# Kernel optimization log

Hardware: AMD Instinct MI355X
Metric: run time of the kernel (lower is better)

Reference implementation:

```python
import jax, jax.numpy as jnp
import numpy as np

B, N1, N2, D, L, H = 2, 384, 384, 128, 3, 128
DM_MIN = 0.5


def _gat_layer(x, adj, W, Wb, A, gW, gb):
    # GAT_gate from jaechanglim/DTI_PDBbind: attention softmax over dim 1, gated residual
    h = x @ W + Wb                                   # [B,N,D]
    e = jnp.einsum('bjl,bkl->bjk', h @ A, h)
    e = e + jnp.swapaxes(e, 1, 2)
    att = jnp.where(adj > 0, e, -9e15)
    att = jax.nn.softmax(att, axis=1) * adj
    h_prime = jax.nn.relu(jnp.einsum('bij,bjk->bik', att, h))
    coeff = jax.nn.sigmoid(jnp.concatenate([x, h_prime], -1) @ gW + gb)  # [B,N,1]
    return coeff * x + (1.0 - coeff) * h_prime


def _pair_mlp(h1g, h2g, W1, b1, W2, b2):
    # MLP(concat(h1_i, h2_j)) without materializing the [B,N1,N2,2D] concat:
    # split W1 into ligand / protein halves and broadcast-add the projections.
    p1 = jnp.einsum('bnd,dk->bnk', h1g, W1[:D])      # [B,N1,H]
    p2 = jnp.einsum('bmd,dk->bmk', h2g, W1[D:])      # [B,N2,H]
    hid = jax.nn.relu(p1[:, :, None, :] + p2[:, None, :, :] + b1)  # [B,N1,N2,H]
    return (hid @ W2 + b2)[..., 0]                   # [B,N1,N2]


def reference(h1, adj1, h2, dmv, charge1, charge2, vdw_epsilon, vdw_sigma,
              delta_uff, valid1, valid2, no_metal1, no_metal2,
              node_W, gat_W, gat_Wb, gat_A, gat_gW, gat_gb,
              pair_W1, pair_b1, pair_W2, pair_b2,
              vdw_coeff, duff_coeff, int_W1, int_b1, int_W2, int_b2):
    h1g = h1 @ node_W
    h2g = h2 @ node_W
    for i in range(L):  # only ligand graph is convolved (as in the source)
        h1g = _gat_layer(h1g, adj1, gat_W[i], gat_Wb[i], gat_A[i], gat_gW[i], gat_gb[i])

    dm = jnp.sqrt(jnp.sum(dmv * dmv, -1) + 1e-10)    # [B,N1,N2]
    dm = jnp.where(dm < DM_MIN, 1e10, dm)

    # coulomb term (pair MLPs 0,1)
    cA = jax.nn.sigmoid(_pair_mlp(h1g, h2g, pair_W1[0], pair_b1[0], pair_W2[0], pair_b2[0]))
    cN = jax.nn.sigmoid(_pair_mlp(h1g, h2g, pair_W1[1], pair_b1[1], pair_W2[1], pair_b2[1])) * 2.0 + 1.0
    charge12 = charge1[:, :, None] * charge2[:, None, :]
    e_c = cA * charge12 * jnp.power(1.0 / dm, cN)
    e_c = e_c * valid1[:, :, None] * valid2[:, None, :]
    e_c = jnp.clip(e_c, -100.0, 100.0)
    e_c = jnp.sum(e_c, axis=(1, 2))[:, None]

    # vdw term (pair MLPs 2=A sigmoid, 3=B tanh, 4=N sigmoid)
    vA = (jax.nn.sigmoid(_pair_mlp(h1g, h2g, pair_W1[2], pair_b1[2], pair_W2[2], pair_b2[2])) * 0.6 + 0.7)
    vA = vA * (vdw_coeff[0] * vdw_coeff[0]) * vdw_epsilon
    vB = jnp.tanh(_pair_mlp(h1g, h2g, pair_W1[3], pair_b1[3], pair_W2[3], pair_b2[3])) * 0.6 + 0.7
    vN = jax.nn.sigmoid(_pair_mlp(h1g, h2g, pair_W1[4], pair_b1[4], pair_W2[4], pair_b2[4])) * 2.0 + 5.0
    dm0 = vdw_sigma * vB
    dm0 = jnp.where(dm0 < 1e-4, 1.0, dm0)
    r = jnp.power(dm0 / dm, vN)
    e_v = vA * (r * r - 2.0 * r)                     # (dm0/dm)^(2N) - 2(dm0/dm)^N
    e_v = e_v * no_metal1[:, :, None] * no_metal2[:, None, :]
    e_v = jnp.minimum(e_v, 100.0)
    e_v = jnp.sum(e_v, axis=(1, 2))[:, None]

    # conformational energy difference term
    e_u = (duff_coeff[0] * duff_coeff[0] * delta_uff)[:, None]

    # learned intercept from pooled ligand features
    hs = jnp.sum(h1g * valid1[..., None], axis=1)
    inter = jax.nn.relu(hs @ int_W1 + int_b1) @ int_W2 + int_b2

    return jnp.concatenate([e_c, e_v, e_u, inter], -1)  # [B,4]


def setup_inputs() -> dict:
    key = jax.random.key(0)
    ks = jax.random.split(key, 24)
    inp = {}
    inp['h1'] = jax.random.normal(ks[0], (B, N1, 54), jnp.float32)
    inp['h2'] = jax.random.normal(ks[1], (B, N2, 54), jnp.float32)
    a = jax.random.uniform(ks[2], (B, N1, N1))
    adj = (a > 0.9).astype(jnp.float32)
    adj = jnp.maximum(adj, jnp.swapaxes(adj, 1, 2))
    inp['adj1'] = jnp.maximum(adj, jnp.eye(N1, dtype=jnp.float32)[None])
    inp['dmv'] = jax.random.normal(ks[3], (B, N1, N2, 3), jnp.float32) * 3.0
    inp['charge1'] = jax.random.normal(ks[4], (B, N1), jnp.float32) * 0.3
    inp['charge2'] = jax.random.normal(ks[5], (B, N2), jnp.float32) * 0.3
    inp['vdw_epsilon'] = jax.random.uniform(ks[6], (B, N1, N2), jnp.float32) * 0.3
    inp['vdw_sigma'] = 3.0 + jax.random.uniform(ks[7], (B, N1, N2), jnp.float32)
    inp['delta_uff'] = jax.random.uniform(ks[8], (B,), jnp.float32) * 5.0
    inp['valid1'] = jnp.ones((B, N1), jnp.float32)
    inp['valid2'] = jnp.ones((B, N2), jnp.float32)
    inp['no_metal1'] = jnp.ones((B, N1), jnp.float32)
    inp['no_metal2'] = jnp.ones((B, N2), jnp.float32)
    # parameters
    inp['node_W'] = jax.random.normal(ks[9], (54, D), jnp.float32) * 0.1
    inp['gat_W'] = jax.random.normal(ks[10], (L, D, D), jnp.float32) * (1.0 / np.sqrt(D))
    inp['gat_Wb'] = jnp.zeros((L, D), jnp.float32)
    inp['gat_A'] = jax.random.normal(ks[11], (L, D, D), jnp.float32) * 0.05
    inp['gat_gW'] = jax.random.normal(ks[12], (L, 2 * D, 1), jnp.float32) * 0.05
    inp['gat_gb'] = jnp.zeros((L, 1), jnp.float32)
    inp['pair_W1'] = jax.random.normal(ks[13], (5, 2 * D, H), jnp.float32) * 0.05
    inp['pair_b1'] = jnp.zeros((5, H), jnp.float32)
    inp['pair_W2'] = jax.random.normal(ks[14], (5, H, 1), jnp.float32) * 0.1
    inp['pair_b2'] = jnp.zeros((5, 1), jnp.float32)
    inp['vdw_coeff'] = jnp.array([0.02], jnp.float32)
    inp['duff_coeff'] = jnp.array([0.1], jnp.float32)
    inp['int_W1'] = jax.random.normal(ks[15], (D, H), jnp.float32) * 0.05
    inp['int_b1'] = jnp.zeros((H,), jnp.float32)
    inp['int_W2'] = jax.random.normal(ks[16], (H, 1), jnp.float32) * 0.1
    inp['int_b2'] = jnp.zeros((1,), jnp.float32)
    return inp
```

## Files before the change

### kernel.cpp

```cpp
#include <hip/hip_runtime.h>
#include <math.h>

#define NN 384
#define DD 128
#define HH 128

__device__ __forceinline__ float sigmoidf_(float x) { return 1.f / (1.f + __expf(-x)); }
__device__ __forceinline__ float tanhf_(float x)    { return 1.f - 2.f / (__expf(2.f * x) + 1.f); }

__global__ __launch_bounds__(256) void k_start(
    const float* __restrict__ h1, const float* __restrict__ h2,
    const float* __restrict__ nW,
    const float* __restrict__ W, const float* __restrict__ Wb, const float* __restrict__ A,
    const float* __restrict__ delta_uff, const float* __restrict__ duff,
    float* __restrict__ h1g, float* __restrict__ h2g,
    float* __restrict__ hb, float* __restrict__ hAb,
    float* __restrict__ hT, float* __restrict__ hAT,
    float* __restrict__ out) {
  int blk = blockIdx.x, tid = threadIdx.x, c = tid & 127, g = tid >> 7;
  if (blk == 0 && tid < 8) {
    int bb = tid >> 2, cc = tid & 3;
    out[tid] = (cc == 2) ? duff[0] * duff[0] * delta_uff[bb] : 0.f;
  }
  if (blk < 384) {
    int r = blk * 2 + g;
    const float* xr = h1 + r * 54;
    float acc = 0.f;
#pragma unroll 6
    for (int k = 0; k < 54; ++k) acc += xr[k] * nW[k * DD + c];
    h1g[r * DD + c] = acc;
    __syncthreads();
    const float4* xr4 = (const float4*)(h1g + r * DD);
    float a0 = 0.f, a1 = 0.f;
#pragma unroll 4
    for (int k4 = 0; k4 < DD / 4; ++k4) {
      float4 xv = xr4[k4]; int k = 4 * k4;
      a0 += xv.x * W[k * DD + c] + xv.z * W[(k + 2) * DD + c];
      a1 += xv.y * W[(k + 1) * DD + c] + xv.w * W[(k + 3) * DD + c];
    }
    float hv = a0 + a1 + Wb[c];
    hb[r * DD + c] = hv; hT[c * 768 + r] = hv;
    __syncthreads();
    const float4* hr4 = (const float4*)(hb + r * DD);
    a0 = 0.f; a1 = 0.f;
#pragma unroll 4
    for (int k4 = 0; k4 < DD / 4; ++k4) {
      float4 xv = hr4[k4]; int k = 4 * k4;
      a0 += xv.x * A[k * DD + c] + xv.z * A[(k + 2) * DD + c];
      a1 += xv.y * A[(k + 1) * DD + c] + xv.w * A[(k + 3) * DD + c];
    }
    float av = a0 + a1;
    hAb[r * DD + c] = av; hAT[c * 768 + r] = av;
  } else {
    int r = (blk - 384) * 2 + g;
    const float* xr = h2 + r * 54;
    float acc = 0.f;
#pragma unroll 6
    for (int k = 0; k < 54; ++k) acc += xr[k] * nW[k * DD + c];
    h2g[r * DD + c] = acc;
  }
}

__global__ __launch_bounds__(384) void k_att(
    const float* __restrict__ hb, const float* __restrict__ hAb,
    const float* __restrict__ hT, const float* __restrict__ hAT,
    const float* __restrict__ adj, float* __restrict__ att) {
  int col = blockIdx.x;
  int b = col / NN, k = col - b * NN;
  int tid = threadIdx.x;
  float a = adj[col * NN + tid];
  const float* hrow  = hb  + col * DD;
  const float* harow = hAb + col * DD;
  const float* hTb   = hT  + b * NN + tid;
  const float* hATb  = hAT + b * NN + tid;
  float e0 = 0.f, e1 = 0.f, e2 = 0.f, e3 = 0.f;
#pragma unroll 4
  for (int cc = 0; cc < DD; cc += 4) {
    e0 += hATb[cc * 768] * hrow[cc] + hTb[cc * 768] * harow[cc];
    e1 += hATb[(cc + 1) * 768] * hrow[cc + 1] + hTb[(cc + 1) * 768] * harow[cc + 1];
    e2 += hATb[(cc + 2) * 768] * hrow[cc + 2] + hTb[(cc + 2) * 768] * harow[cc + 2];
    e3 += hATb[(cc + 3) * 768] * hrow[cc + 3] + hTb[(cc + 3) * 768] * harow[cc + 3];
  }
  float e = (e0 + e1) + (e2 + e3);
  __shared__ float red[6];
  float lmax = (a > 0.f) ? e : -3e38f;
#pragma unroll
  for (int off = 32; off > 0; off >>= 1) lmax = fmaxf(lmax, __shfl_down(lmax, off));
  int w = tid >> 6;
  if ((tid & 63) == 0) red[w] = lmax;
  __syncthreads();
  float m = red[0];
#pragma unroll
  for (int q = 1; q < 6; ++q) m = fmaxf(m, red[q]);
  float v = (a > 0.f) ? __expf(e - m) : 0.f;
  float s = v;
#pragma unroll
  for (int off = 32; off > 0; off >>= 1) s += __shfl_down(s, off);
  __syncthreads();
  if ((tid & 63) == 0) red[w] = s;
  __syncthreads();
  float d = 0.f;
#pragma unroll
  for (int q = 0; q < 6; ++q) d += red[q];
  att[(b * NN + tid) * NN + k] = v * a / d;
}

__global__ __launch_bounds__(256) void k_out_hhA(
    const float* __restrict__ x, const float* __restrict__ hb,
    const float* __restrict__ att,
    const float* __restrict__ gW, const float* __restrict__ gb,
    const float* __restrict__ Wn, const float* __restrict__ Wbn,
    const float* __restrict__ An,
    float* __restrict__ xout,
    float* __restrict__ hbn, float* __restrict__ hAbn,
    float* __restrict__ hTn, float* __restrict__ hATn) {
  int r = blockIdx.x;
  int b = r / NN;
  int tid = threadIdx.x, c = tid & 127, jh = tid >> 7;
  __shared__ float ph[2][DD];
  __shared__ float redw[2];
  float xr = x[r * DD + c];
  float g1 = gW[c], g2 = gW[DD + c], gbv = gb[0];
  const float4* ar4 = (const float4*)(att + r * NN) + jh * 48;
  const float* hp = hb + (b * NN + jh * 192) * DD + c;
  float q0 = 0.f, q1 = 0.f, q2 = 0.f, q3 = 0.f;
#pragma unroll 4
  for (int j4 = 0; j4 < 48; ++j4) {
    float4 av = ar4[j4];
    const float* hj = hp + j4 * 4 * DD;
    q0 += av.x * hj[0];
    q1 += av.y * hj[DD];
    q2 += av.z * hj[2 * DD];
    q3 += av.w * hj[3 * DD];
  }
  ph[jh][c] = (q0 + q1) + (q2 + q3);
  __syncthreads();
  float hpr = 0.f;
  if (tid < 128) {
    hpr = fmaxf(ph[0][c] + ph[1][c], 0.f);
    float v = xr * g1 + hpr * g2;
#pragma unroll
    for (int off = 32; off > 0; off >>= 1) v += __shfl_down(v, off);
    if ((tid & 63) == 0) redw[tid >> 6] = v;
  }
  __syncthreads();
  if (tid < 128) {
    float coeff = sigmoidf_(redw[0] + redw[1] + gbv);
    xout[r * DD + c] = coeff * xr + (1.f - coeff) * hpr;
  }
  __syncthreads();
  const float* xb = xout + r * DD + jh * 64;
  const float* Wp = Wn + (jh * 64) * DD + c;
  float a0 = 0.f, a1 = 0.f;
#pragma unroll 4
  for (int k = 0; k < 64; k += 2) {
    a0 += xb[k] * Wp[k * DD];
    a1 += xb[k + 1] * Wp[(k + 1) * DD];
  }
  ph[jh][c] = a0 + a1;
  __syncthreads();
  if (tid < 128) {
    float hv = ph[0][c] + ph[1][c] + Wbn[c];
    hbn[r * DD + c] = hv; hTn[c * 768 + r] = hv;
  }
  __syncthreads();
  const float* hbr = hbn + r * DD + jh * 64;
  const float* Ap = An + (jh * 64) * DD + c;
  a0 = 0.f; a1 = 0.f;
#pragma unroll 4
  for (int k = 0; k < 64; k += 2) {
    a0 += hbr[k] * Ap[k * DD];
    a1 += hbr[k + 1] * Ap[(k + 1) * DD];
  }
  ph[jh][c] = a0 + a1;
  __syncthreads();
  if (tid < 128) {
    float av = ph[0][c] + ph[1][c];
    hAbn[r * DD + c] = av; hATn[c * 768 + r] = av;
  }
}

__global__ __launch_bounds__(256) void k_out_proj(
    const float* __restrict__ x, const float* __restrict__ hb,
    const float* __restrict__ att,
    const float* __restrict__ gW, const float* __restrict__ gb,
    const float* __restrict__ pW1, const float* __restrict__ pb1,
    const float* __restrict__ valid1, const float* __restrict__ h2g,
    float* __restrict__ xout, float* __restrict__ p1, float* __restrict__ p2q,
    float* __restrict__ wsi) {
  int blk = blockIdx.x, tid = threadIdx.x, c = tid & 127, jh = tid >> 7;
  if (blk >= 768) {
    int rp = blk - 768;
    const float* xbase = h2g + rp * DD;
    for (int o = tid; o < 640; o += 256) {
      int m = o >> 7, hc = o & 127;
      const float* Wcol = pW1 + (m * 256 + 128) * HH + hc;
      float a0 = 0.f, a1 = 0.f;
#pragma unroll 4
      for (int k = 0; k < DD; k += 2) {
        a0 += xbase[k] * Wcol[k * HH];
        a1 += xbase[k + 1] * Wcol[(k + 1) * HH];
      }
      p2q[(size_t)((m * 32 + (hc >> 2)) * 768 + rp) * 4 + (hc & 3)] = a0 + a1;
    }
    return;
  }
  int r = blk;
  int b = r / NN;
  __shared__ float ph[2][DD];
  __shared__ float redw[2];
  float xr = x[r * DD + c];
  float g1 = gW[c], g2 = gW[DD + c], gbv = gb[0];
  float vld = valid1[r];
  const float4* ar4 = (const float4*)(att + r * NN) + jh * 48;
  const float* hp = hb + (b * NN + jh * 192) * DD + c;
  float q0 = 0.f, q1 = 0.f, q2 = 0.f, q3 = 0.f;
#pragma unroll 4
  for (int j4 = 0; j4 < 48; ++j4) {
    float4 av = ar4[j4];
    const float* hj = hp + j4 * 4 * DD;
    q0 += av.x * hj[0];
    q1 += av.y * hj[DD];
    q2 += av.z * hj[2 * DD];
    q3 += av.w * hj[3 * DD];
  }
  ph[jh][c] = (q0 + q1) + (q2 + q3);
  __syncthreads();
  float hpr = 0.f;
  if (tid < 128) {
    hpr = fmaxf(ph[0][c] + ph[1][c], 0.f);
    float v = xr * g1 + hpr * g2;
#pragma unroll
    for (int off = 32; off > 0; off >>= 1) v += __shfl_down(v, off);
    if ((tid & 63) == 0) redw[tid >> 6] = v;
  }
  __syncthreads();
  if (tid < 128) {
    float coeff = sigmoidf_(redw[0] + redw[1] + gbv);
    float nv = coeff * xr + (1.f - coeff) * hpr;
    xout[r * DD + c] = nv;
    wsi[r * DD + c] = nv * vld;
  }
  __syncthreads();
  const float* xbase = xout + r * DD;
  for (int o = tid; o < 640; o += 256) {
    int m = o >> 7, hc = o & 127;
    const float* Wcol = pW1 + (m * 256) * HH + hc;
    float a0 = 0.f, a1 = 0.f;
#pragma unroll 4
    for (int k = 0; k < DD; k += 2) {
      a0 += xbase[k] * Wcol[k * HH];
      a1 += xbase[k + 1] * Wcol[(k + 1) * HH];
    }
    p1[(r * 5 + m) * HH + hc] = a0 + a1 + pb1[m * HH + hc];
  }
}

__global__ __launch_bounds__(384) void k_energy(
    const float* __restrict__ p1, const float* __restrict__ p2q,
    const float* __restrict__ W2, const float* __restrict__ b2,
    const float* __restrict__ dmv, const float* __restrict__ charge1,
    const float* __restrict__ charge2, const float* __restrict__ veps,
    const float* __restrict__ vsig, const float* __restrict__ valid1,
    const float* __restrict__ valid2, const float* __restrict__ nm1,
    const float* __restrict__ nm2, const float* __restrict__ vdw_coeff,
    const float* __restrict__ wsi, const float* __restrict__ iW1,
    const float* __restrict__ ib1, const float* __restrict__ iW2,
    const float* __restrict__ ib2, float* __restrict__ out) {
  int blk = blockIdx.x, tid = threadIdx.x;
  if (blk >= 384) {
    if (tid < 256) {
      int bb = tid >> 7, cc = tid & 127;
      __shared__ float hsf[2][DD];
      __shared__ float redf[2][2];
      float a0 = 0.f, a1 = 0.f;
      for (int q = 0; q < 384; q += 2) {
        a0 += wsi[(bb * 384 + q) * DD + cc];
        a1 += wsi[(bb * 384 + q + 1) * DD + cc];
      }
      hsf[bb][cc] = a0 + a1;
      __syncthreads();
      float hid = ib1[cc];
#pragma unroll 4
      for (int k = 0; k < DD; ++k) hid += hsf[bb][k] * iW1[k * HH + cc];
      hid = fmaxf(hid, 0.f);
      float v = hid * iW2[cc];
#pragma unroll
      for (int off = 32; off > 0; off >>= 1) v += __shfl_down(v, off);
      if ((tid & 63) == 0) redf[bb][(tid >> 6) & 1] = v;
      __syncthreads();
      if (tid < 2) out[tid * 4 + 3] = redf[tid][0] + redf[tid][1] + ib2[0];
    }
    return;
  }
  int r0 = blk * 2;
  int b = r0 / NN;
  int j = tid;
  int col = b * NN + j;
  int p0 = r0 * NN + j, pI = p0 + NN;
  float dx0 = dmv[3 * p0], dy0 = dmv[3 * p0 + 1], dz0 = dmv[3 * p0 + 2];
  float dx1 = dmv[3 * pI], dy1 = dmv[3 * pI + 1], dz1 = dmv[3 * pI + 2];
  float ve0 = veps[p0], ve1 = veps[pI];
  float vs0 = vsig[p0], vs1 = vsig[pI];
  float q2c = charge2[col], vv2 = valid2[col], n2 = nm2[col];
  float c1a = charge1[r0], c1b = charge1[r0 + 1];
  float vaa = valid1[r0], vab = valid1[r0 + 1];
  float naa = nm1[r0], nab = nm1[r0 + 1];
  float vc2 = vdw_coeff[0] * vdw_coeff[0];

  const float* q0 = p1 + (r0 + 0) * 640;
  const float* q1 = p1 + (r0 + 1) * 640;
  const float4* p2q4 = (const float4*)p2q;
  float acc0[5], acc1[5];
#pragma unroll
  for (int m = 0; m < 5; ++m) {
    const float4* pc = p2q4 + (size_t)(m * 32) * 768 + col;
    const float* x0m = q0 + m * HH;
    const float* x1m = q1 + m * HH;
    const float* w2m = W2 + m * HH;
    float a0 = 0.f, a1 = 0.f;
#pragma unroll 8
    for (int hq = 0; hq < 32; ++hq) {
      float4 pv = pc[(size_t)hq * 768];
      float w0 = w2m[4 * hq], w1 = w2m[4 * hq + 1];
      float w2v = w2m[4 * hq + 2], w3 = w2m[4 * hq + 3];
      a0 += fmaxf(x0m[4 * hq] + pv.x, 0.f) * w0 + fmaxf(x0m[4 * hq + 1] + pv.y, 0.f) * w1
          + fmaxf(x0m[4 * hq + 2] + pv.z, 0.f) * w2v + fmaxf(x0m[4 * hq + 3] + pv.w, 0.f) * w3;
      a1 += fmaxf(x1m[4 * hq] + pv.x, 0.f) * w0 + fmaxf(x1m[4 * hq + 1] + pv.y, 0.f) * w1
          + fmaxf(x1m[4 * hq + 2] + pv.z, 0.f) * w2v + fmaxf(x1m[4 * hq + 3] + pv.w, 0.f) * w3;
    }
    acc0[m] = a0 + b2[m]; acc1[m] = a1 + b2[m];
  }

  float ec_sum = 0.f, ev_sum = 0.f;
  {
    float dm = sqrtf(dx0 * dx0 + dy0 * dy0 + dz0 * dz0 + 1e-10f);
    if (dm < 0.5f) dm = 1e10f;
    float cA = sigmoidf_(acc0[0]);
    float cN = sigmoidf_(acc0[1]) * 2.f + 1.f;
    float e_c = cA * c1a * q2c * __powf(1.f / dm, cN);
    e_c *= vaa * vv2;
    ec_sum += fminf(fmaxf(e_c, -100.f), 100.f);
    float vA = (sigmoidf_(acc0[2]) * 0.6f + 0.7f) * vc2 * ve0;
    float vB = tanhf_(acc0[3]) * 0.6f + 0.7f;
    float vN = sigmoidf_(acc0[4]) * 2.f + 5.f;
    float dm0 = vs0 * vB;
    if (dm0 < 1e-4f) dm0 = 1.f;
    float rr = __powf(dm0 / dm, vN);
    float e_v = vA * (rr * rr - 2.f * rr) * naa * n2;
    ev_sum += fminf(e_v, 100.f);
  }
  {
    float dm = sqrtf(dx1 * dx1 + dy1 * dy1 + dz1 * dz1 + 1e-10f);
    if (dm < 0.5f) dm = 1e10f;
    float cA = sigmoidf_(acc1[0]);
    float cN = sigmoidf_(acc1[1]) * 2.f + 1.f;
    float e_c = cA * c1b * q2c * __powf(1.f / dm, cN);
    e_c *= vab * vv2;
    ec_sum += fminf(fmaxf(e_c, -100.f), 100.f);
    float vA = (sigmoidf_(acc1[2]) * 0.6f + 0.7f) * vc2 * ve1;
    float vB = tanhf_(acc1[3]) * 0.6f + 0.7f;
    float vN = sigmoidf_(acc1[4]) * 2.f + 5.f;
    float dm0 = vs1 * vB;
    if (dm0 < 1e-4f) dm0 = 1.f;
    float rr = __powf(dm0 / dm, vN);
    float e_v = vA * (rr * rr - 2.f * rr) * nab * n2;
    ev_sum += fminf(e_v, 100.f);
  }
#pragma unroll
  for (int off = 32; off > 0; off >>= 1) {
    ec_sum += __shfl_down(ec_sum, off);
    ev_sum += __shfl_down(ev_sum, off);
  }
  __shared__ float rec[6], rev[6];
  if ((tid & 63) == 0) { rec[tid >> 6] = ec_sum; rev[tid >> 6] = ev_sum; }
  __syncthreads();
  if (tid == 0) {
    float a = 0.f, c = 0.f;
#pragma unroll
    for (int w = 0; w < 6; ++w) { a += rec[w]; c += rev[w]; }
    atomicAdd(&out[b * 4 + 0], a);
    atomicAdd(&out[b * 4 + 1], c);
  }
}

extern "C" void kernel_launch(void* const* d_in, const int* in_sizes, int n_in,
                              void* d_out, int out_size, void* d_ws, size_t ws_size,
                              hipStream_t stream) {
  (void)in_sizes; (void)n_in; (void)out_size; (void)ws_size;
  const float* h1         = (const float*)d_in[0];
  const float* h2         = (const float*)d_in[1];
  const float* adj1       = (const float*)d_in[2];
  const float* dmv        = (const float*)d_in[3];
  const float* charge1    = (const float*)d_in[4];
  const float* charge2    = (const float*)d_in[5];
  const float* veps       = (const float*)d_in[6];
  const float* vsig       = (const float*)d_in[7];
  const float* delta_uff  = (const float*)d_in[8];
  const float* valid1     = (const float*)d_in[9];
  const float* valid2     = (const float*)d_in[10];
  const float* nm1        = (const float*)d_in[11];
  const float* nm2        = (const float*)d_in[12];
  const float* node_W     = (const float*)d_in[13];
  const float* gat_W      = (const float*)d_in[14];
  const float* gat_Wb     = (const float*)d_in[15];
  const float* gat_A      = (const float*)d_in[16];
  const float* gat_gW     = (const float*)d_in[17];
  const float* gat_gb     = (const float*)d_in[18];
  const float* pW1        = (const float*)d_in[19];
  const float* pb1        = (const float*)d_in[20];
  const float* pW2        = (const float*)d_in[21];
  const float* pb2        = (const float*)d_in[22];
  const float* vdw_coeff  = (const float*)d_in[23];
  const float* duff_coeff = (const float*)d_in[24];
  const float* iW1        = (const float*)d_in[25];
  const float* ib1        = (const float*)d_in[26];
  const float* iW2        = (const float*)d_in[27];
  const float* ib2        = (const float*)d_in[28];
  float* out = (float*)d_out;

  float* ws = (float*)d_ws;
  const int RN = 768 * DD;
  float* h1gA = ws;
  float* h1gB = h1gA + RN;
  float* h2g  = h1gB + RN;
  float* hb0  = h2g  + RN;
  float* hA0  = hb0  + RN;
  float* hT0  = hA0  + RN;
  float* hAT0 = hT0  + RN;
  float* hb1  = hAT0 + RN;
  float* hA1  = hb1  + RN;
  float* hT1  = hA1  + RN;
  float* hAT1 = hT1  + RN;
  float* att  = hAT1 + RN;
  float* p1   = att + 2 * NN * NN;
  float* p2q  = p1 + 768 * 640;
  float* wsi  = p2q + 768 * 640;

  const int DD2 = DD * DD;

  k_start<<<dim3(768), dim3(256), 0, stream>>>(
      h1, h2, node_W, gat_W, gat_Wb, gat_A, delta_uff, duff_coeff,
      h1gA, h2g, hb0, hA0, hT0, hAT0, out);

  k_att<<<dim3(768), dim3(384), 0, stream>>>(hb0, hA0, hT0, hAT0, adj1, att);
  k_out_hhA<<<dim3(768), dim3(256), 0, stream>>>(
      h1gA, hb0, att, gat_gW + 0, gat_gb + 0,
      gat_W + DD2, gat_Wb + DD, gat_A + DD2,
      h1gB, hb1, hA1, hT1, hAT1);
  k_att<<<dim3(768), dim3(384), 0, stream>>>(hb1, hA1, hT1, hAT1, adj1, att);
  k_out_hhA<<<dim3(768), dim3(256), 0, stream>>>(
      h1gB, hb1, att, gat_gW + 2 * DD, gat_gb + 1,
      gat_W + 2 * DD2, gat_Wb + 2 * DD, gat_A + 2 * DD2,
      h1gA, hb0, hA0, hT0, hAT0);
  k_att<<<dim3(768), dim3(384), 0, stream>>>(hb0, hA0, hT0, hAT0, adj1, att);
  k_out_proj<<<dim3(1536), dim3(256), 0, stream>>>(
      h1gA, hb0, att, gat_gW + 4 * DD, gat_gb + 2,
      pW1, pb1, valid1, h2g, h1gB, p1, p2q, wsi);

  k_energy<<<dim3(385), dim3(384), 0, stream>>>(
      p1, p2q, pW2, pb2, dmv, charge1, charge2, veps, vsig,
      valid1, valid2, nm1, nm2, vdw_coeff, wsi, iW1, ib1, iW2, ib2, out);
}
```

Measured before the change: 285.3 us.

## Process two rows/columns per block in GAT attention and projection kernels

Each block in k_att, k_out_hhA and k_out_proj now handles two adjacent rows (or columns) instead of one, and the grid sizes are halved to match. Each loaded element of hT/hAT, hb and the weight columns is reused for two outputs, which cuts global/L2 traffic per output and launch count. In k_att the attention output is written as a float2. In exchange there are fewer blocks (384 on a large GPU) and more registers per thread, which lowers parallelism and occupancy.

```diff
diff --git a/kernel.cpp b/kernel.cpp
--- a/kernel.cpp
+++ b/kernel.cpp
@@ -65,44 +65,60 @@
     const float* __restrict__ hb, const float* __restrict__ hAb,
     const float* __restrict__ hT, const float* __restrict__ hAT,
     const float* __restrict__ adj, float* __restrict__ att) {
-  int col = blockIdx.x;
-  int b = col / NN, k = col - b * NN;
+  int blk = blockIdx.x;
+  int b = blk / 192;
+  int kk = (blk - b * 192) * 2;
+  int col0 = b * NN + kk, col1 = col0 + 1;
   int tid = threadIdx.x;
-  float a = adj[col * NN + tid];
-  const float* hrow  = hb  + col * DD;
-  const float* harow = hAb + col * DD;
-  const float* hTb   = hT  + b * NN + tid;
-  const float* hATb  = hAT + b * NN + tid;
-  float e0 = 0.f, e1 = 0.f, e2 = 0.f, e3 = 0.f;
-#pragma unroll 4
-  for (int cc = 0; cc < DD; cc += 4) {
-    e0 += hATb[cc * 768] * hrow[cc] + hTb[cc * 768] * harow[cc];
-    e1 += hATb[(cc + 1) * 768] * hrow[cc + 1] + hTb[(cc + 1) * 768] * harow[cc + 1];
-    e2 += hATb[(cc + 2) * 768] * hrow[cc + 2] + hTb[(cc + 2) * 768] * harow[cc + 2];
-    e3 += hATb[(cc + 3) * 768] * hrow[cc + 3] + hTb[(cc + 3) * 768] * harow[cc + 3];
-  }
-  float e = (e0 + e1) + (e2 + e3);
-  __shared__ float red[6];
-  float lmax = (a > 0.f) ? e : -3e38f;
-#pragma unroll
-  for (int off = 32; off > 0; off >>= 1) lmax = fmaxf(lmax, __shfl_down(lmax, off));
+  float a0 = adj[col0 * NN + tid];
+  float a1 = adj[col1 * NN + tid];
+  const float* h0r = hb  + col0 * DD;
+  const float* g0r = hAb + col0 * DD;
+  const float* h1r = hb  + col1 * DD;
+  const float* g1r = hAb + col1 * DD;
+  const float* hTb  = hT  + b * NN + tid;
+  const float* hATb = hAT + b * NN + tid;
+  float e0a = 0.f, e0b = 0.f, e1a = 0.f, e1b = 0.f;
+#pragma unroll 4
+  for (int cc = 0; cc < DD; cc += 2) {
+    float tv0 = hTb[cc * 768], av0 = hATb[cc * 768];
+    float tv1 = hTb[(cc + 1) * 768], av1 = hATb[(cc + 1) * 768];
+    e0a += av0 * h0r[cc] + tv0 * g0r[cc];
+    e0b += av1 * h0r[cc + 1] + tv1 * g0r[cc + 1];
+    e1a += av0 * h1r[cc] + tv0 * g1r[cc];
+    e1b += av1 * h1r[cc + 1] + tv1 * g1r[cc + 1];
+  }
+  float e0 = e0a + e0b, e1 = e1a + e1b;
+  __shared__ float red[2][6];
+  float l0 = (a0 > 0.f) ? e0 : -3e38f;
+  float l1 = (a1 > 0.f) ? e1 : -3e38f;
+#pragma unroll
+  for (int off = 32; off > 0; off >>= 1) {
+    l0 = fmaxf(l0, __shfl_down(l0, off));
+    l1 = fmaxf(l1, __shfl_down(l1, off));
+  }
   int w = tid >> 6;
-  if ((tid & 63) == 0) red[w] = lmax;
-  __syncthreads();
-  float m = red[0];
-#pragma unroll
-  for (int q = 1; q < 6; ++q) m = fmaxf(m, red[q]);
-  float v = (a > 0.f) ? __expf(e - m) : 0.f;
-  float s = v;
-#pragma unroll
-  for (int off = 32; off > 0; off >>= 1) s += __shfl_down(s, off);
-  __syncthreads();
-  if ((tid & 63) == 0) red[w] = s;
-  __syncthreads();
-  float d = 0.f;
-#pragma unroll
-  for (int q = 0; q < 6; ++q) d += red[q];
-  att[(b * NN + tid) * NN + k] = v * a / d;
+  if ((tid & 63) == 0) { red[0][w] = l0; red[1][w] = l1; }
+  __syncthreads();
+  float m0 = red[0][0], m1 = red[1][0];
+#pragma unroll
+  for (int q = 1; q < 6; ++q) { m0 = fmaxf(m0, red[0][q]); m1 = fmaxf(m1, red[1][q]); }
+  float v0 = (a0 > 0.f) ? __expf(e0 - m0) : 0.f;
+  float v1 = (a1 > 0.f) ? __expf(e1 - m1) : 0.f;
+  float s0 = v0, s1 = v1;
+#pragma unroll
+  for (int off = 32; off > 0; off >>= 1) {
+    s0 += __shfl_down(s0, off);
+    s1 += __shfl_down(s1, off);
+  }
+  __syncthreads();
+  if ((tid & 63) == 0) { red[0][w] = s0; red[1][w] = s1; }
+  __syncthreads();
+  float d0 = 0.f, d1 = 0.f;
+#pragma unroll
+  for (int q = 0; q < 6; ++q) { d0 += red[0][q]; d1 += red[1][q]; }
+  float2 wv = make_float2(v0 * a0 / d0, v1 * a1 / d1);
+  *(float2*)(att + (b * NN + tid) * NN + kk) = wv;
 }
 
 __global__ __launch_bounds__(256) void k_out_hhA(
@@ -114,69 +130,91 @@
     float* __restrict__ xout,
     float* __restrict__ hbn, float* __restrict__ hAbn,
     float* __restrict__ hTn, float* __restrict__ hATn) {
-  int r = blockIdx.x;
-  int b = r / NN;
+  int r0 = blockIdx.x * 2;
+  int b = r0 / NN;
   int tid = threadIdx.x, c = tid & 127, jh = tid >> 7;
-  __shared__ float ph[2][DD];
-  __shared__ float redw[2];
-  float xr = x[r * DD + c];
+  __shared__ float ph[2][2][DD];
+  __shared__ float redw[2][2];
+  float xr0 = x[(r0 + 0) * DD + c];
+  float xr1 = x[(r0 + 1) * DD + c];
   float g1 = gW[c], g2 = gW[DD + c], gbv = gb[0];
-  const float4* ar4 = (const float4*)(att + r * NN) + jh * 48;
+  const float4* a0p = (const float4*)(att + (r0 + 0) * NN) + jh * 48;
+  const float4* a1p = (const float4*)(att + (r0 + 1) * NN) + jh * 48;
   const float* hp = hb + (b * NN + jh * 192) * DD + c;
-  float q0 = 0.f, q1 = 0.f, q2 = 0.f, q3 = 0.f;
+  float q00 = 0.f, q01 = 0.f, q10 = 0.f, q11 = 0.f;
 #pragma unroll 4
   for (int j4 = 0; j4 < 48; ++j4) {
-    float4 av = ar4[j4];
+    float4 av0 = a0p[j4], av1 = a1p[j4];
     const float* hj = hp + j4 * 4 * DD;
-    q0 += av.x * hj[0];
-    q1 += av.y * hj[DD];
-    q2 += av.z * hj[2 * DD];
-    q3 += av.w * hj[3 * DD];
-  }
-  ph[jh][c] = (q0 + q1) + (q2 + q3);
-  __syncthreads();
-  float hpr = 0.f;
+    float h0 = hj[0], h1v = hj[DD], h2v = hj[2 * DD], h3 = hj[3 * DD];
+    q00 += av0.x * h0 + av0.y * h1v;
+    q01 += av0.z * h2v + av0.w * h3;
+    q10 += av1.x * h0 + av1.y * h1v;
+    q11 += av1.z * h2v + av1.w * h3;
+  }
+  ph[jh][0][c] = q00 + q01;
+  ph[jh][1][c] = q10 + q11;
+  __syncthreads();
+  float hpr0 = 0.f, hpr1 = 0.f;
   if (tid < 128) {
-    hpr = fmaxf(ph[0][c] + ph[1][c], 0.f);
-    float v = xr * g1 + hpr * g2;
-#pragma unroll
-    for (int off = 32; off > 0; off >>= 1) v += __shfl_down(v, off);
-    if ((tid & 63) == 0) redw[tid >> 6] = v;
+    hpr0 = fmaxf(ph[0][0][c] + ph[1][0][c], 0.f);
+    hpr1 = fmaxf(ph[0][1][c] + ph[1][1][c], 0.f);
+    float v0 = xr0 * g1 + hpr0 * g2;
+    float v1 = xr1 * g1 + hpr1 * g2;
+#pragma unroll
+    for (int off = 32; off > 0; off >>= 1) {
+      v0 += __shfl_down(v0, off);
+      v1 += __shfl_down(v1, off);
+    }
+    if ((tid & 63) == 0) { redw[0][tid >> 6] = v0; redw[1][tid >> 6] = v1; }
   }
   __syncthreads();
   if (tid < 128) {
-    float coeff = sigmoidf_(redw[0] + redw[1] + gbv);
-    xout[r * DD + c] = coeff * xr + (1.f - coeff) * hpr;
-  }
-  __syncthreads();
-  const float* xb = xout + r * DD + jh * 64;
+    float c0 = sigmoidf_(redw[0][0] + redw[0][1] + gbv);
+    float c1 = sigmoidf_(redw[1][0] + redw[1][1] + gbv);
+    xout[(r0 + 0) * DD + c] = c0 * xr0 + (1.f - c0) * hpr0;
+    xout[(r0 + 1) * DD + c] = c1 * xr1 + (1.f - c1) * hpr1;
+  }
+  __syncthreads();
+  const float* xb0 = xout + (r0 + 0) * DD + jh * 64;
+  const float* xb1 = xout + (r0 + 1) * DD + jh * 64;
   const float* Wp = Wn + (jh * 64) * DD + c;
-  float a0 = 0.f, a1 = 0.f;
+  float a00 = 0.f, a01 = 0.f, a10 = 0.f, a11 = 0.f;
 #pragma unroll 4
   for (int k = 0; k < 64; k += 2) {
-    a0 += xb[k] * Wp[k * DD];
-    a1 += xb[k + 1] * Wp[(k + 1) * DD];
-  }
-  ph[jh][c] = a0 + a1;
+    float w0 = Wp[k * DD], w1 = Wp[(k + 1) * DD];
+    a00 += xb0[k] * w0; a01 += xb0[k + 1] * w1;
+    a10 += xb1[k] * w0; a11 += xb1[k + 1] * w1;
+  }
+  ph[jh][0][c] = a00 + a01;
+  ph[jh][1][c] = a10 + a11;
   __syncthreads();
   if (tid < 128) {
-    float hv = ph[0][c] + ph[1][c] + Wbn[c];
-    hbn[r * DD + c] = hv; hTn[c * 768 + r] = hv;
-  }
-  __syncthreads();
-  const float* hbr = hbn + r * DD + jh * 64;
+    float wb = Wbn[c];
+    float hv0 = ph[0][0][c] + ph[1][0][c] + wb;
+    float hv1 = ph[0][1][c] + ph[1][1][c] + wb;
+    hbn[(r0 + 0) * DD + c] = hv0; hTn[c * 768 + r0 + 0] = hv0;
+    hbn[(r0 + 1) * DD + c] = hv1; hTn[c * 768 + r0 + 1] = hv1;
+  }
+  __syncthreads();
+  const float* hb0p = hbn + (r0 + 0) * DD + jh * 64;
+  const float* hb1p = hbn + (r0 + 1) * DD + jh * 64;
   const float* Ap = An + (jh * 64) * DD + c;
-  a0 = 0.f; a1 = 0.f;
+  a00 = 0.f; a01 = 0.f; a10 = 0.f; a11 = 0.f;
 #pragma unroll 4
   for (int k = 0; k < 64; k += 2) {
-    a0 += hbr[k] * Ap[k * DD];
-    a1 += hbr[k + 1] * Ap[(k + 1) * DD];
-  }
-  ph[jh][c] = a0 + a1;
+    float w0 = Ap[k * DD], w1 = Ap[(k + 1) * DD];
+    a00 += hb0p[k] * w0; a01 += hb0p[k + 1] * w1;
+    a10 += hb1p[k] * w0; a11 += hb1p[k + 1] * w1;
+  }
+  ph[jh][0][c] = a00 + a01;
+  ph[jh][1][c] = a10 + a11;
   __syncthreads();
   if (tid < 128) {
-    float av = ph[0][c] + ph[1][c];
-    hAbn[r * DD + c] = av; hATn[c * 768 + r] = av;
+    float av0 = ph[0][0][c] + ph[1][0][c];
+    float av1 = ph[0][1][c] + ph[1][1][c];
+    hAbn[(r0 + 0) * DD + c] = av0; hATn[c * 768 + r0 + 0] = av0;
+    hAbn[(r0 + 1) * DD + c] = av1; hATn[c * 768 + r0 + 1] = av1;
   }
 }
 
@@ -189,70 +227,91 @@
     float* __restrict__ xout, float* __restrict__ p1, float* __restrict__ p2q,
     float* __restrict__ wsi) {
   int blk = blockIdx.x, tid = threadIdx.x, c = tid & 127, jh = tid >> 7;
-  if (blk >= 768) {
-    int rp = blk - 768;
-    const float* xbase = h2g + rp * DD;
+  if (blk >= 384) {
+    int rp = (blk - 384) * 2;
+    const float* xb0 = h2g + (rp + 0) * DD;
+    const float* xb1 = h2g + (rp + 1) * DD;
     for (int o = tid; o < 640; o += 256) {
       int m = o >> 7, hc = o & 127;
       const float* Wcol = pW1 + (m * 256 + 128) * HH + hc;
-      float a0 = 0.f, a1 = 0.f;
+      float a00 = 0.f, a01 = 0.f, a10 = 0.f, a11 = 0.f;
 #pragma unroll 4
       for (int k = 0; k < DD; k += 2) {
-        a0 += xbase[k] * Wcol[k * HH];
-        a1 += xbase[k + 1] * Wcol[(k + 1) * HH];
+        float w0 = Wcol[k * HH], w1 = Wcol[(k + 1) * HH];
+        a00 += xb0[k] * w0; a01 += xb0[k + 1] * w1;
+        a10 += xb1[k] * w0; a11 += xb1[k + 1] * w1;
       }
-      p2q[(size_t)((m * 32 + (hc >> 2)) * 768 + rp) * 4 + (hc & 3)] = a0 + a1;
+      float* dst = p2q + (size_t)((m * 32 + (hc >> 2)) * 768 + rp) * 4 + (hc & 3);
+      dst[0] = a00 + a01;
+      dst[4] = a10 + a11;
     }
     return;
   }
-  int r = blk;
-  int b = r / NN;
-  __shared__ float ph[2][DD];
-  __shared__ float redw[2];
-  float xr = x[r * DD + c];
+  int r0 = blk * 2;
+  int b = r0 / NN;
+  __shared__ float ph[2][2][DD];
+  __shared__ float redw[2][2];
+  float xr0 = x[(r0 + 0) * DD + c];
+  float xr1 = x[(r0 + 1) * DD + c];
   float g1 = gW[c], g2 = gW[DD + c], gbv = gb[0];
-  float vld = valid1[r];
-  const float4* ar4 = (const float4*)(att + r * NN) + jh * 48;
+  float vld0 = valid1[r0], vld1 = valid1[r0 + 1];
+  const float4* a0p = (const float4*)(att + (r0 + 0) * NN) + jh * 48;
+  const float4* a1p = (const float4*)(att + (r0 + 1) * NN) + jh * 48;
   const float* hp = hb + (b * NN + jh * 192) * DD + c;
-  float q0 = 0.f, q1 = 0.f, q2 = 0.f, q3 = 0.f;
+  float q00 = 0.f, q01 = 0.f, q10 = 0.f, q11 = 0.f;
 #pragma unroll 4
   for (int j4 = 0; j4 < 48; ++j4) {
-    float4 av = ar4[j4];
+    float4 av0 = a0p[j4], av1 = a1p[j4];
     const float* hj = hp + j4 * 4 * DD;
-    q0 += av.x * hj[0];
-    q1 += av.y * hj[DD];
-    q2 += av.z * hj[2 * DD];
-    q3 += av.w * hj[3 * DD];
-  }
-  ph[jh][c] = (q0 + q1) + (q2 + q3);
-  __syncthreads();
-  float hpr = 0.f;
+    float h0 = hj[0], h1v = hj[DD], h2v = hj[2 * DD], h3 = hj[3 * DD];
+    q00 += av0.x * h0 + av0.y * h1v;
+    q01 += av0.z * h2v + av0.w * h3;
+    q10 += av1.x * h0 + av1.y * h1v;
+    q11 += av1.z * h2v + av1.w * h3;
+  }
+  ph[jh][0][c] = q00 + q01;
+  ph[jh][1][c] = q10 + q11;
+  __syncthreads();
+  float hpr0 = 0.f, hpr1 = 0.f;
   if (tid < 128) {
-    hpr = fmaxf(ph[0][c] + ph[1][c], 0.f);
-    float v = xr * g1 + hpr * g2;
-#pragma unroll
-    for (int off = 32; off > 0; off >>= 1) v += __shfl_down(v, off);
-    if ((tid & 63) == 0) redw[tid >> 6] = v;
+    hpr0 = fmaxf(ph[0][0][c] + ph[1][0][c], 0.f);
+    hpr1 = fmaxf(ph[0][1][c] + ph[1][1][c], 0.f);
+    float v0 = xr0 * g1 + hpr0 * g2;
+    float v1 = xr1 * g1 + hpr1 * g2;
+#pragma unroll
+    for (int off = 32; off > 0; off >>= 1) {
+      v0 += __shfl_down(v0, off);
+      v1 += __shfl_down(v1, off);
+    }
+    if ((tid & 63) == 0) { redw[0][tid >> 6] = v0; redw[1][tid >> 6] = v1; }
   }
   __syncthreads();
   if (tid < 128) {
-    float coeff = sigmoidf_(redw[0] + redw[1] + gbv);
-    float nv = coeff * xr + (1.f - coeff) * hpr;
-    xout[r * DD + c] = nv;
-    wsi[r * DD + c] = nv * vld;
-  }
-  __syncthreads();
-  const float* xbase = xout + r * DD;
+    float c0 = sigmoidf_(redw[0][0] + redw[0][1] + gbv);
+    float c1 = sigmoidf_(redw[1][0] + redw[1][1] + gbv);
+    float nv0 = c0 * xr0 + (1.f - c0) * hpr0;
+    float nv1 = c1 * xr1 + (1.f - c1) * hpr1;
+    xout[(r0 + 0) * DD + c] = nv0;
+    xout[(r0 + 1) * DD + c] = nv1;
+    wsi[(r0 + 0) * DD + c] = nv0 * vld0;
+    wsi[(r0 + 1) * DD + c] = nv1 * vld1;
+  }
+  __syncthreads();
+  const float* xb0 = xout + (r0 + 0) * DD;
+  const float* xb1 = xout + (r0 + 1) * DD;
   for (int o = tid; o < 640; o += 256) {
     int m = o >> 7, hc = o & 127;
     const float* Wcol = pW1 + (m * 256) * HH + hc;
-    float a0 = 0.f, a1 = 0.f;
+    float a00 = 0.f, a01 = 0.f, a10 = 0.f, a11 = 0.f;
 #pragma unroll 4
     for (int k = 0; k < DD; k += 2) {
-      a0 += xbase[k] * Wcol[k * HH];
-      a1 += xbase[k + 1] * Wcol[(k + 1) * HH];
-    }
-    p1[(r * 5 + m) * HH + hc] = a0 + a1 + pb1[m * HH + hc];
+      float w0 = Wcol[k * HH], w1 = Wcol[(k + 1) * HH];
+      a00 += xb0[k] * w0; a01 += xb0[k + 1] * w1;
+      a10 += xb1[k] * w0; a11 += xb1[k + 1] * w1;
+    }
+    float bias = pb1[m * HH + hc];
+    p1[((r0 + 0) * 5 + m) * HH + hc] = a00 + a01 + bias;
+    p1[((r0 + 1) * 5 + m) * HH + hc] = a10 + a11 + bias;
   }
 }
 
@@ -443,18 +502,18 @@
       h1, h2, node_W, gat_W, gat_Wb, gat_A, delta_uff, duff_coeff,
       h1gA, h2g, hb0, hA0, hT0, hAT0, out);
 
-  k_att<<<dim3(768), dim3(384), 0, stream>>>(hb0, hA0, hT0, hAT0, adj1, att);
-  k_out_hhA<<<dim3(768), dim3(256), 0, stream>>>(
+  k_att<<<dim3(384), dim3(384), 0, stream>>>(hb0, hA0, hT0, hAT0, adj1, att);
+  k_out_hhA<<<dim3(384), dim3(256), 0, stream>>>(
       h1gA, hb0, att, gat_gW + 0, gat_gb + 0,
       gat_W + DD2, gat_Wb + DD, gat_A + DD2,
       h1gB, hb1, hA1, hT1, hAT1);
-  k_att<<<dim3(768), dim3(384), 0, stream>>>(hb1, hA1, hT1, hAT1, adj1, att);
-  k_out_hhA<<<dim3(768), dim3(256), 0, stream>>>(
+  k_att<<<dim3(384), dim3(384), 0, stream>>>(hb1, hA1, hT1, hAT1, adj1, att);
+  k_out_hhA<<<dim3(384), dim3(256), 0, stream>>>(
       h1gB, hb1, att, gat_gW + 2 * DD, gat_gb + 1,
       gat_W + 2 * DD2, gat_Wb + 2 * DD, gat_A + 2 * DD2,
       h1gA, hb0, hA0, hT0, hAT0);
-  k_att<<<dim3(768), dim3(384), 0, stream>>>(hb0, hA0, hT0, hAT0, adj1, att);
-  k_out_proj<<<dim3(1536), dim3(256), 0, stream>>>(
+  k_att<<<dim3(384), dim3(384), 0, stream>>>(hb0, hA0, hT0, hAT0, adj1, att);
+  k_out_proj<<<dim3(768), dim3(256), 0, stream>>>(
       h1gA, hb0, att, gat_gW + 4 * DD, gat_gb + 2,
       pW1, pb1, valid1, h2g, h1gB, p1, p2q, wsi);
 
```

Result: faster. 267.0 us (-6.4%).
